# Performance work log

Measured on AMD Instinct MI355X. Metric: run time of the kernel, lower is better.

## Reference

```python
import jax, jax.numpy as jnp
import numpy as np

NUM_HEADS = 16

def setup_inputs() -> dict:
    key = jax.random.key(0)
    ks = jax.random.split(key, 6)
    b, t, d = 2, 2048, 1024
    s = 0.02
    return {
        "x": jax.random.normal(ks[0], (b, t, d), jnp.float32),
        "Wq": jax.random.normal(ks[1], (d, d), jnp.float32) * s,
        "Wk": jax.random.normal(ks[2], (d, d), jnp.float32) * s,
        "Wv": jax.random.normal(ks[3], (d, d), jnp.float32) * s,
        "Wo": jax.random.normal(ks[4], (d, d), jnp.float32) * s,
        "bo": jnp.zeros((d,), jnp.float32),
    }

def reference(x, Wq, Wk, Wv, Wo, bo):
    b, t, d = x.shape
    h = NUM_HEADS
    hd = d // h  # head_dim = d_out / num_heads
    # torch nn.Linear: y = x @ W.T (qkv_bias=False)
    def split_heads(y):
        return y.reshape(b, t, h, hd).transpose(0, 2, 1, 3)  # [b,h,t,hd]
    q = split_heads(x @ Wq.T)
    k = split_heads(x @ Wk.T)
    v = split_heads(x @ Wv.T)
    scale = 1.0 / jnp.sqrt(jnp.asarray(hd, x.dtype))
    # NOTE: original forward computes but never applies the causal mask or dropout
    scores = jnp.einsum('bhqd,bhkd->bhqk', q, k) * scale
    attn = jax.nn.softmax(scores, axis=-1)
    ctx = jnp.einsum('bhqk,bhkd->bhqd', attn, v)
    ctx = ctx.transpose(0, 2, 1, 3).reshape(b, t, d)
    return ctx @ Wo.T + bo
```

## Files before the change

### kernel.cpp

```cpp
#include <hip/hip_runtime.h>
#include <hip/hip_bf16.h>
#include <math.h>
#include <stdint.h>
#include <string.h>

#define TSEQ 2048
#define DMODEL 1024
#define NH 16
#define HD 64
#define BROWS 4096
#define BH 32

typedef __attribute__((ext_vector_type(8))) short short8;
typedef __attribute__((ext_vector_type(4))) float floatx4;

#define MFMA16 __builtin_amdgcn_mfma_f32_16x16x32_bf16
#define SWZ8(r, q) ((((q) ^ ((r) & 7)) * 8))

#define QSCALE 0.18033688011112042f

__device__ __forceinline__ unsigned short bf16_rne(float f) {
    uint32_t u = __float_as_uint(f);
    u += 0x7FFFu + ((u >> 16) & 1u);
    return (unsigned short)(u >> 16);
}

__device__ __forceinline__ uint32_t pack_bf16x2(float a, float b) {
    __hip_bfloat162 h = __float22bfloat162_rn(float2{a, b});
    uint32_t r;
    memcpy(&r, &h, 4);
    return r;
}

__device__ __forceinline__ void split_bf16(float f, short& hi, short& lo) {
    uint32_t u = __float_as_uint(f);
    hi = (short)(u >> 16);
    float hif = __uint_as_float(u & 0xFFFF0000u);
    lo = (short)bf16_rne(f - hif);
}

__device__ __forceinline__ void async16(const void* g, void* l) {
    __builtin_amdgcn_global_load_lds(
        (__attribute__((address_space(1))) const uint32_t*)g,
        (__attribute__((address_space(3))) uint32_t*)l, 16, 0, 0);
}

struct PackArgs {
    const float4* x;
    ushort4* xb;
    const float4* w[3];
    ushort4* wb[3];
    const float4* wo;
    ushort4* woh;
    ushort4* wol;
};
__global__ __launch_bounds__(256) void pack_all(PackArgs a) {
    const int y = blockIdx.y;
    const int base = blockIdx.x * 256 + threadIdx.x;
    if (y == 0) {
#pragma unroll
        for (int it = 0; it < 4; ++it) {
            int i = base + it * 262144;
            float4 f = a.x[i];
            a.xb[i] = make_ushort4(bf16_rne(f.x), bf16_rne(f.y),
                                   bf16_rne(f.z), bf16_rne(f.w));
        }
    } else if (y <= 3) {
        int w = y - 1;
        float4 f = a.w[w][base];
        a.wb[w][base] = make_ushort4(bf16_rne(f.x), bf16_rne(f.y),
                                     bf16_rne(f.z), bf16_rne(f.w));
    } else {
        float4 f = a.wo[base];
        short h0, l0, h1, l1, h2, l2, h3, l3;
        split_bf16(f.x, h0, l0); split_bf16(f.y, h1, l1);
        split_bf16(f.z, h2, l2); split_bf16(f.w, h3, l3);
        a.woh[base] = make_ushort4(h0, h1, h2, h3);
        a.wol[base] = make_ushort4(l0, l1, l2, l3);
    }
}

__global__ __launch_bounds__(256) void gemm_qkv(
    const short* __restrict__ Xb,
    const short* __restrict__ Bq, const short* __restrict__ Bk,
    const short* __restrict__ Bv,
    short* __restrict__ Qo, short* __restrict__ Ko, short* __restrict__ Vo) {
    __shared__ short sA[128 * 64];
    __shared__ short sB[128 * 64];
    const int K = DMODEL;

    const int tid = threadIdx.x;
    const int lane = tid & 63, wave = tid >> 6;
    const int quad = lane >> 4, col = lane & 15;
    const int m0 = blockIdx.y * 128, n0 = blockIdx.x * 128;
    const int which = n0 >> 10;
    const int nn0 = n0 & 1023;
    const int wm = wave >> 1, wn = wave & 1;

    const short* B = (which == 0) ? Bq : (which == 1) ? Bk : Bv;
    const short* Asrc = Xb + (size_t)m0 * K;
    const short* Bsrc = B + (size_t)nn0 * K;

    const int srow = lane >> 3;
    const int soff = (((lane & 7) ^ srow) * 8);

    floatx4 acc[4][4] = {};

    for (int k0 = 0; k0 < K; k0 += 64) {
        __syncthreads();
#pragma unroll
        for (int j = 0; j < 8; ++j) {
            int idx = wave * 8 + j;
            int sub = idx & 15;
            const short* s = (idx < 16) ? Asrc : Bsrc;
            short* d = (idx < 16) ? sA : sB;
            async16(s + (size_t)(sub * 8 + srow) * K + k0 + soff, d + sub * 512);
        }
        __syncthreads();

#pragma unroll
        for (int s2 = 0; s2 < 2; ++s2) {
            short8 a_b[4], b_b[4];
#pragma unroll
            for (int mi = 0; mi < 4; ++mi) {
                int r = wm * 64 + mi * 16 + col;
                a_b[mi] = *(const short8*)&sA[r * 64 + SWZ8(r, s2 * 4 + quad)];
            }
#pragma unroll
            for (int ni = 0; ni < 4; ++ni) {
                int r = wn * 64 + ni * 16 + col;
                b_b[ni] = *(const short8*)&sB[r * 64 + SWZ8(r, s2 * 4 + quad)];
            }
            if (which == 2) {
#pragma unroll
                for (int mi = 0; mi < 4; ++mi)
#pragma unroll
                    for (int ni = 0; ni < 4; ++ni)
                        acc[mi][ni] = MFMA16(a_b[mi], b_b[ni], acc[mi][ni], 0, 0, 0);
            } else {
#pragma unroll
                for (int mi = 0; mi < 4; ++mi)
#pragma unroll
                    for (int ni = 0; ni < 4; ++ni)
                        acc[mi][ni] = MFMA16(b_b[ni], a_b[mi], acc[mi][ni], 0, 0, 0);
            }
        }
    }

    const int mb = m0 + wm * 64;
    const int nlb = nn0 + wn * 64;
    if (which == 2) {
#pragma unroll
        for (int ni = 0; ni < 4; ++ni) {
            int n = nlb + ni * 16 + col;
            int h = n >> 6, hd = n & 63;
#pragma unroll
            for (int mi = 0; mi < 4; ++mi) {
                int m4 = mb + mi * 16 + quad * 4;
                int b = m4 >> 11, t0 = m4 & 2047;
                int sw = (t0 & 32) | ((t0 & 12) << 1) | ((t0 & 16) >> 2);
                int tsw = (t0 & ~63) | ((((sw >> 3) ^ (hd & 7)) << 3) | (sw & 7));
                size_t row = ((size_t)(b * NH + h) * HD + hd) * TSEQ;
                *(ushort4*)&Vo[row + tsw] =
                    make_ushort4(bf16_rne(acc[mi][ni][0]), bf16_rne(acc[mi][ni][1]),
                                 bf16_rne(acc[mi][ni][2]), bf16_rne(acc[mi][ni][3]));
            }
        }
    } else {
        short* O = (which == 0) ? Qo : Ko;
        const float sc = (which == 0) ? QSCALE : 1.0f;
#pragma unroll
        for (int mi = 0; mi < 4; ++mi) {
            int m = mb + mi * 16 + col;
            int b = m >> 11, t = m & 2047;
#pragma unroll
            for (int ni = 0; ni < 4; ++ni) {
                int n = nlb + ni * 16 + quad * 4;
                int h = n >> 6, hd = n & 63;
                int hds = (which == 1) ? ((((hd >> 3) ^ (t & 7)) << 3) | (hd & 7)) : hd;
                size_t idx = ((size_t)(b * NH + h) * TSEQ + t) * HD + hds;
                *(ushort4*)&O[idx] =
                    make_ushort4(bf16_rne(acc[mi][ni][0] * sc), bf16_rne(acc[mi][ni][1] * sc),
                                 bf16_rne(acc[mi][ni][2] * sc), bf16_rne(acc[mi][ni][3] * sc));
            }
        }
    }
}

#define ATTN_COMPUTE(DB)                                                        \
    {                                                                           \
        _Pragma("unroll")                                                       \
        for (int u = 0; u < 2; ++u) {                                           \
            floatx4 s[4] = {};                                                  \
            __builtin_amdgcn_s_setprio(1);                                      \
            _Pragma("unroll")                                                   \
            for (int k4 = 0; k4 < 4; ++k4) {                                    \
                short8 kf0 = *(const short8*)(kb0 + (DB) * 8192 + u * 4096 + k4 * 1024); \
                short8 kf1 = *(const short8*)(kb1 + (DB) * 8192 + u * 4096 + k4 * 1024); \
                s[k4] = MFMA16(kf0, qf[0], s[k4], 0, 0, 0);                     \
                s[k4] = MFMA16(kf1, qf[1], s[k4], 0, 0, 0);                     \
            }                                                                   \
            __builtin_amdgcn_s_setprio(0);                                      \
            float p[4][4];                                                      \
            _Pragma("unroll")                                                   \
            for (int k4 = 0; k4 < 4; ++k4)                                      \
                _Pragma("unroll")                                               \
                for (int r4 = 0; r4 < 4; ++r4)                                  \
                    p[k4][r4] = __builtin_amdgcn_exp2f(s[k4][r4]);              \
            _Pragma("unroll")                                                   \
            for (int c = 0; c < 2; ++c) {                                       \
                union { short8 v; uint32_t w[4]; } pf;                          \
                pf.w[0] = pack_bf16x2(p[2 * c][0], p[2 * c][1]);                \
                pf.w[1] = pack_bf16x2(p[2 * c][2], p[2 * c][3]);                \
                pf.w[2] = pack_bf16x2(p[2 * c + 1][0], p[2 * c + 1][1]);        \
                pf.w[3] = pack_bf16x2(p[2 * c + 1][2], p[2 * c + 1][3]);        \
                const short* vbc = c ? vb1 : vb0;                               \
                __builtin_amdgcn_s_setprio(1);                                  \
                lacc = MFMA16(ones.v, pf.v, lacc, 0, 0, 0);                     \
                _Pragma("unroll")                                               \
                for (int ni = 0; ni < 4; ++ni) {                                \
                    short8 vf = *(const short8*)(vbc + (DB) * 8192 + u * 4096 + ni * 1024); \
                    O[ni] = MFMA16(vf, pf.v, O[ni], 0, 0, 0);                   \
                }                                                               \
                __builtin_amdgcn_s_setprio(0);                                  \
            }                                                                   \
        }                                                                       \
    }

#define STAGE(LB)                                                               \
    {                                                                           \
        async16(g0, (LB) + 0 * 512);                                            \
        async16(g1, (LB) + 1 * 512);                                            \
        async16(g2, (LB) + 2 * 512);                                            \
        async16(g3, (LB) + 3 * 512);                                            \
        g0 += ktstep; g1 += ktstep; g2 += ktstep; g3 += ktstep;                 \
    }

__global__ __launch_bounds__(512, 4) void attn_bf16(
    const short* __restrict__ Qb, const short* __restrict__ Kb,
    const short* __restrict__ Vb, short* __restrict__ Cb) {
    __shared__ short sK[2][2][64 * 64];
    __shared__ short sV[2][2][64 * 64];

    const int tid = threadIdx.x;
    const int lane = tid & 63, wave = tid >> 6;
    const int quad = lane >> 4, col = lane & 15;
    const int qt = blockIdx.x, bh = blockIdx.y;
    const size_t bhoff = (size_t)bh * TSEQ * HD;

    const size_t qrow = (size_t)(qt * 128 + wave * 16 + col) * HD;
    short8 qf[2];
#pragma unroll
    for (int c = 0; c < 2; ++c)
        qf[c] = *(const short8*)&Qb[bhoff + qrow + c * 32 + quad * 8];

    const int srow = lane >> 3;
    const int schunk = (lane & 7) * 8;

    const int isV = wave >> 2;
    const int tl = (wave >> 1) & 1;
    const int sb = (wave & 1) * 4;

    const short *g0, *g1, *g2, *g3;
    size_t ktstep;
    if (!isV) {
        g0 = Kb + bhoff + (size_t)(tl * 64 + (sb + 0) * 8 + srow) * HD + schunk;
        g1 = Kb + bhoff + (size_t)(tl * 64 + (sb + 1) * 8 + srow) * HD + schunk;
        g2 = Kb + bhoff + (size_t)(tl * 64 + (sb + 2) * 8 + srow) * HD + schunk;
        g3 = Kb + bhoff + (size_t)(tl * 64 + (sb + 3) * 8 + srow) * HD + schunk;
        ktstep = (size_t)128 * HD;
    } else {
        g0 = Vb + bhoff + (size_t)((sb + 0) * 8 + srow) * TSEQ + tl * 64 + schunk;
        g1 = Vb + bhoff + (size_t)((sb + 1) * 8 + srow) * TSEQ + tl * 64 + schunk;
        g2 = Vb + bhoff + (size_t)((sb + 2) * 8 + srow) * TSEQ + tl * 64 + schunk;
        g3 = Vb + bhoff + (size_t)((sb + 3) * 8 + srow) * TSEQ + tl * 64 + schunk;
        ktstep = 128;
    }
    short* lb0_ = isV ? &sV[0][tl][sb * 512] : &sK[0][tl][sb * 512];
    short* lb1_ = isV ? &sV[1][tl][sb * 512] : &sK[1][tl][sb * 512];

    const int ch0 = ((quad ^ (col & 7)) << 3);
    const int ch1 = (((4 + quad) ^ (col & 7)) << 3);
    const short* kb0 = &sK[0][0][col * 64 + ch0];
    const short* kb1 = &sK[0][0][col * 64 + ch1];
    const short* vb0 = &sV[0][0][col * 64 + ch0];
    const short* vb1 = &sV[0][0][col * 64 + ch1];

    union { short8 v; short s[8]; } ones;
#pragma unroll
    for (int j = 0; j < 8; ++j) ones.s[j] = (short)0x3F80;

    floatx4 lacc = {};
    floatx4 O[4] = {};

    STAGE(lb0_);

    for (int kt2 = 0; kt2 < 8; ++kt2) {
        STAGE(lb1_);
        asm volatile("s_waitcnt vmcnt(4)" ::: "memory");
        __builtin_amdgcn_s_barrier();
        ATTN_COMPUTE(0);
        __builtin_amdgcn_s_barrier();

        if (kt2 < 7) {
            STAGE(lb0_);
            asm volatile("s_waitcnt vmcnt(4)" ::: "memory");
        } else {
            asm volatile("s_waitcnt vmcnt(0)" ::: "memory");
        }
        __builtin_amdgcn_s_barrier();
        ATTN_COMPUTE(1);
        __builtin_amdgcn_s_barrier();
    }

    const float inv = 1.0f / lacc[0];

    const int b = bh >> 4, h = bh & 15;
    const int trow = qt * 128 + wave * 16 + col;
    const size_t obase = (size_t)(b * TSEQ + trow) * DMODEL + h * 64;
#pragma unroll
    for (int ni = 0; ni < 4; ++ni) {
        uint2 pk;
        pk.x = pack_bf16x2(O[ni][0] * inv, O[ni][1] * inv);
        pk.y = pack_bf16x2(O[ni][2] * inv, O[ni][3] * inv);
        *(uint2*)&Cb[obase + ni * 16 + quad * 4] = pk;
    }
}

__global__ __launch_bounds__(256) void gemm_out(
    const short* __restrict__ Ab,
    const short* __restrict__ Bh, const short* __restrict__ Bl,
    const float* __restrict__ bias, float* __restrict__ Of) {
    __shared__ short sA[128 * 64];
    __shared__ short sBh[64 * 64];
    __shared__ short sBl[64 * 64];
    const int K = DMODEL, N = DMODEL;

    const int tid = threadIdx.x;
    const int lane = tid & 63, wave = tid >> 6;
    const int quad = lane >> 4, col = lane & 15;
    const int m0 = blockIdx.y * 128, n0 = blockIdx.x * 64;
    const int wm = wave >> 1, wn = wave & 1;

    const short* Asrc = Ab + (size_t)m0 * K;
    const short* Bhsrc = Bh + (size_t)n0 * K;
    const short* Blsrc = Bl + (size_t)n0 * K;
    const int srow = lane >> 3;
    const int soff = (((lane & 7) ^ srow) * 8);

    floatx4 acc[4][2] = {};

    for (int k0 = 0; k0 < K; k0 += 64) {
        __syncthreads();
#pragma unroll
        for (int j = 0; j < 8; ++j) {
            int idx = wave * 8 + j;
            int buf = (idx < 16) ? 0 : (idx < 24) ? 1 : 2;
            int sub = (buf == 0) ? idx : (buf == 1) ? idx - 16 : idx - 24;
            const short* s = (buf == 0) ? Asrc : (buf == 1) ? Bhsrc : Blsrc;
            short* d = (buf == 0) ? sA : (buf == 1) ? sBh : sBl;
            async16(s + (size_t)(sub * 8 + srow) * K + k0 + soff, d + sub * 512);
        }
        __syncthreads();

#pragma unroll
        for (int s2 = 0; s2 < 2; ++s2) {
            short8 a_b[4], b_h[2], b_l[2];
#pragma unroll
            for (int mi = 0; mi < 4; ++mi) {
                int r = wm * 64 + mi * 16 + col;
                a_b[mi] = *(const short8*)&sA[r * 64 + SWZ8(r, s2 * 4 + quad)];
            }
#pragma unroll
            for (int ni = 0; ni < 2; ++ni) {
                int r = wn * 32 + ni * 16 + col;
                b_h[ni] = *(const short8*)&sBh[r * 64 + SWZ8(r, s2 * 4 + quad)];
                b_l[ni] = *(const short8*)&sBl[r * 64 + SWZ8(r, s2 * 4 + quad)];
            }
#pragma unroll
            for (int mi = 0; mi < 4; ++mi)
#pragma unroll
                for (int ni = 0; ni < 2; ++ni) {
                    acc[mi][ni] = MFMA16(b_h[ni], a_b[mi], acc[mi][ni], 0, 0, 0);
                    acc[mi][ni] = MFMA16(b_l[ni], a_b[mi], acc[mi][ni], 0, 0, 0);
                }
        }
    }

    const int mb = m0 + wm * 64, nb = n0 + wn * 32;
#pragma unroll
    for (int mi = 0; mi < 4; ++mi) {
        int m = mb + mi * 16 + col;
#pragma unroll
        for (int ni = 0; ni < 2; ++ni) {
            int n = nb + ni * 16 + quad * 4;
            float4 bv = *(const float4*)&bias[n];
            float4 o = make_float4(acc[mi][ni][0] + bv.x, acc[mi][ni][1] + bv.y,
                                   acc[mi][ni][2] + bv.z, acc[mi][ni][3] + bv.w);
            *(float4*)&Of[(size_t)m * N + n] = o;
        }
    }
}

extern "C" void kernel_launch(void* const* d_in, const int* in_sizes, int n_in,
                              void* d_out, int out_size, void* d_ws, size_t ws_size,
                              hipStream_t stream) {
    const float* x  = (const float*)d_in[0];
    const float* Wq = (const float*)d_in[1];
    const float* Wk = (const float*)d_in[2];
    const float* Wv = (const float*)d_in[3];
    const float* Wo = (const float*)d_in[4];
    const float* bo = (const float*)d_in[5];
    float* out = (float*)d_out;

    const size_t NX = (size_t)BROWS * DMODEL;
    const size_t NW = (size_t)DMODEL * DMODEL;
    short* p = (short*)d_ws;
    short *xb = p;
    short *wqb = xb + NX;
    short *wkb = wqb + NW;
    short *wvb = wkb + NW;
    short *woh = wvb + NW; short *wol = woh + NW;
    short *qb = wol + NW;
    short *kb = qb + NX;
    short *vb = kb + NX;
    short *cb = vb + NX;

    PackArgs pa;
    pa.x = (const float4*)x; pa.xb = (ushort4*)xb;
    pa.w[0] = (const float4*)Wq; pa.wb[0] = (ushort4*)wqb;
    pa.w[1] = (const float4*)Wk; pa.wb[1] = (ushort4*)wkb;
    pa.w[2] = (const float4*)Wv; pa.wb[2] = (ushort4*)wvb;
    pa.wo = (const float4*)Wo; pa.woh = (ushort4*)woh; pa.wol = (ushort4*)wol;
    pack_all<<<dim3(1024, 5), dim3(256), 0, stream>>>(pa);

    gemm_qkv<<<dim3(3 * DMODEL / 128, BROWS / 128), dim3(256), 0, stream>>>(
        xb, wqb, wkb, wvb, qb, kb, vb);

    attn_bf16<<<dim3(TSEQ / 128, BH), dim3(512), 0, stream>>>(qb, kb, vb, cb);

    gemm_out<<<dim3(DMODEL / 64, BROWS / 128), dim3(256), 0, stream>>>(cb, woh, wol, bo, out);
}
```

Before: 196.4 us.

## Switch attention kernel to 32x32x16 MFMA tiles with 4 waves per block

Rewrites the attention inner loop to use 32x32x16 bf16 MFMA instead of 16x16x32. Each wave now owns 32 query rows, and the block drops from 8 waves to 4. The softmax row sum is now accumulated in VALU and finished with a cross-lane shuffle, replacing the ones-vector MFMA. The V layout swizzle written by the QKV GEMM and the K/V staging loop are changed to match the new fragment layout. Larger MFMA tiles should raise LDS operand reuse and cut instruction count, at the cost of more registers per wave and fewer waves to hide latency.

```diff
diff --git a/kernel.cpp b/kernel.cpp
--- a/kernel.cpp
+++ b/kernel.cpp
@@ -13,8 +13,10 @@
 
 typedef __attribute__((ext_vector_type(8))) short short8;
 typedef __attribute__((ext_vector_type(4))) float floatx4;
+typedef __attribute__((ext_vector_type(16))) float floatx16;
 
 #define MFMA16 __builtin_amdgcn_mfma_f32_16x16x32_bf16
+#define MFMA32 __builtin_amdgcn_mfma_f32_32x32x16_bf16
 #define SWZ8(r, q) ((((q) ^ ((r) & 7)) * 8))
 
 #define QSCALE 0.18033688011112042f
@@ -158,7 +160,7 @@
             for (int mi = 0; mi < 4; ++mi) {
                 int m4 = mb + mi * 16 + quad * 4;
                 int b = m4 >> 11, t0 = m4 & 2047;
-                int sw = (t0 & 32) | ((t0 & 12) << 1) | ((t0 & 16) >> 2);
+                int sw = (t0 & 0x33) | ((t0 & 4) << 1) | ((t0 & 8) >> 1);
                 int tsw = (t0 & ~63) | ((((sw >> 3) ^ (hd & 7)) << 3) | (sw & 7));
                 size_t row = ((size_t)(b * NH + h) * HD + hd) * TSEQ;
                 *(ushort4*)&Vo[row + tsw] =
@@ -189,38 +191,39 @@
 
 #define ATTN_COMPUTE(DB)                                                        \
     {                                                                           \
+        floatx16 s[4] = {};                                                     \
+        __builtin_amdgcn_s_setprio(1);                                          \
         _Pragma("unroll")                                                       \
-        for (int u = 0; u < 2; ++u) {                                           \
-            floatx4 s[4] = {};                                                  \
-            __builtin_amdgcn_s_setprio(1);                                      \
+        for (int u = 0; u < 2; ++u)                                             \
             _Pragma("unroll")                                                   \
-            for (int k4 = 0; k4 < 4; ++k4) {                                    \
-                short8 kf0 = *(const short8*)(kb0 + (DB) * 8192 + u * 4096 + k4 * 1024); \
-                short8 kf1 = *(const short8*)(kb1 + (DB) * 8192 + u * 4096 + k4 * 1024); \
-                s[k4] = MFMA16(kf0, qf[0], s[k4], 0, 0, 0);                     \
-                s[k4] = MFMA16(kf1, qf[1], s[k4], 0, 0, 0);                     \
+            for (int mm = 0; mm < 2; ++mm)                                      \
+                _Pragma("unroll")                                               \
+                for (int ks = 0; ks < 4; ++ks) {                                \
+                    short8 kf = *(const short8*)(kB[ks] + (DB) * 8192 + u * 4096 + mm * 2048); \
+                    s[u * 2 + mm] = MFMA32(kf, qf[ks], s[u * 2 + mm], 0, 0, 0); \
+                }                                                               \
+        __builtin_amdgcn_s_setprio(0);                                          \
+        _Pragma("unroll")                                                       \
+        for (int m = 0; m < 4; ++m) {                                           \
+            float p[16];                                                        \
+            _Pragma("unroll")                                                   \
+            for (int r = 0; r < 16; ++r) {                                      \
+                p[r] = __builtin_amdgcn_exp2f(s[m][r]);                         \
+                lv[r & 3] += p[r];                                              \
             }                                                                   \
-            __builtin_amdgcn_s_setprio(0);                                      \
-            float p[4][4];                                                      \
-            _Pragma("unroll")                                                   \
-            for (int k4 = 0; k4 < 4; ++k4)                                      \
-                _Pragma("unroll")                                               \
-                for (int r4 = 0; r4 < 4; ++r4)                                  \
-                    p[k4][r4] = __builtin_amdgcn_exp2f(s[k4][r4]);              \
             _Pragma("unroll")                                                   \
             for (int c = 0; c < 2; ++c) {                                       \
                 union { short8 v; uint32_t w[4]; } pf;                          \
-                pf.w[0] = pack_bf16x2(p[2 * c][0], p[2 * c][1]);                \
-                pf.w[1] = pack_bf16x2(p[2 * c][2], p[2 * c][3]);                \
-                pf.w[2] = pack_bf16x2(p[2 * c + 1][0], p[2 * c + 1][1]);        \
-                pf.w[3] = pack_bf16x2(p[2 * c + 1][2], p[2 * c + 1][3]);        \
-                const short* vbc = c ? vb1 : vb0;                               \
+                pf.w[0] = pack_bf16x2(p[8 * c + 0], p[8 * c + 1]);              \
+                pf.w[1] = pack_bf16x2(p[8 * c + 2], p[8 * c + 3]);              \
+                pf.w[2] = pack_bf16x2(p[8 * c + 4], p[8 * c + 5]);              \
+                pf.w[3] = pack_bf16x2(p[8 * c + 6], p[8 * c + 7]);              \
+                const int t = m * 2 + c, uu = t >> 2, tt = t & 3;               \
                 __builtin_amdgcn_s_setprio(1);                                  \
-                lacc = MFMA16(ones.v, pf.v, lacc, 0, 0, 0);                     \
                 _Pragma("unroll")                                               \
-                for (int ni = 0; ni < 4; ++ni) {                                \
-                    short8 vf = *(const short8*)(vbc + (DB) * 8192 + u * 4096 + ni * 1024); \
-                    O[ni] = MFMA16(vf, pf.v, O[ni], 0, 0, 0);                   \
+                for (int mi = 0; mi < 2; ++mi) {                                \
+                    short8 vf = *(const short8*)(vB[tt] + (DB) * 8192 + uu * 4096 + mi * 2048); \
+                    O2[mi] = MFMA32(vf, pf.v, O2[mi], 0, 0, 0);                 \
                 }                                                               \
                 __builtin_amdgcn_s_setprio(0);                                  \
             }                                                                   \
@@ -229,14 +232,13 @@
 
 #define STAGE(LB)                                                               \
     {                                                                           \
-        async16(g0, (LB) + 0 * 512);                                            \
-        async16(g1, (LB) + 1 * 512);                                            \
-        async16(g2, (LB) + 2 * 512);                                            \
-        async16(g3, (LB) + 3 * 512);                                            \
-        g0 += ktstep; g1 += ktstep; g2 += ktstep; g3 += ktstep;                 \
-    }
-
-__global__ __launch_bounds__(512, 4) void attn_bf16(
+        _Pragma("unroll")                                                       \
+        for (int j = 0; j < 8; ++j)                                             \
+            async16(gb + (size_t)j * gstride, (LB) + j * 512);                  \
+        gb += ktstep;                                                           \
+    }
+
+__global__ __launch_bounds__(256, 2) void attn_bf16(
     const short* __restrict__ Qb, const short* __restrict__ Kb,
     const short* __restrict__ Vb, short* __restrict__ Cb) {
     __shared__ short sK[2][2][64 * 64];
@@ -244,67 +246,55 @@
 
     const int tid = threadIdx.x;
     const int lane = tid & 63, wave = tid >> 6;
-    const int quad = lane >> 4, col = lane & 15;
+    const int q5 = lane & 31, hh = lane >> 5, l7 = lane & 7;
     const int qt = blockIdx.x, bh = blockIdx.y;
     const size_t bhoff = (size_t)bh * TSEQ * HD;
 
-    const size_t qrow = (size_t)(qt * 128 + wave * 16 + col) * HD;
-    short8 qf[2];
-#pragma unroll
-    for (int c = 0; c < 2; ++c)
-        qf[c] = *(const short8*)&Qb[bhoff + qrow + c * 32 + quad * 8];
-
-    const int srow = lane >> 3;
-    const int schunk = (lane & 7) * 8;
-
-    const int isV = wave >> 2;
-    const int tl = (wave >> 1) & 1;
-    const int sb = (wave & 1) * 4;
-
-    const short *g0, *g1, *g2, *g3;
-    size_t ktstep;
+    const size_t qrow = (size_t)(qt * 128 + wave * 32 + q5) * HD;
+    short8 qf[4];
+#pragma unroll
+    for (int ks = 0; ks < 4; ++ks)
+        qf[ks] = *(const short8*)&Qb[bhoff + qrow + ks * 16 + hh * 8];
+
+    const int srow = lane >> 3, schunk = (lane & 7) * 8;
+    const int isV = wave >> 1, tl = wave & 1;
+    const short* gb;
+    size_t gstride, ktstep;
     if (!isV) {
-        g0 = Kb + bhoff + (size_t)(tl * 64 + (sb + 0) * 8 + srow) * HD + schunk;
-        g1 = Kb + bhoff + (size_t)(tl * 64 + (sb + 1) * 8 + srow) * HD + schunk;
-        g2 = Kb + bhoff + (size_t)(tl * 64 + (sb + 2) * 8 + srow) * HD + schunk;
-        g3 = Kb + bhoff + (size_t)(tl * 64 + (sb + 3) * 8 + srow) * HD + schunk;
+        gb = Kb + bhoff + (size_t)(tl * 64 + srow) * HD + schunk;
+        gstride = (size_t)8 * HD;
         ktstep = (size_t)128 * HD;
     } else {
-        g0 = Vb + bhoff + (size_t)((sb + 0) * 8 + srow) * TSEQ + tl * 64 + schunk;
-        g1 = Vb + bhoff + (size_t)((sb + 1) * 8 + srow) * TSEQ + tl * 64 + schunk;
-        g2 = Vb + bhoff + (size_t)((sb + 2) * 8 + srow) * TSEQ + tl * 64 + schunk;
-        g3 = Vb + bhoff + (size_t)((sb + 3) * 8 + srow) * TSEQ + tl * 64 + schunk;
+        gb = Vb + bhoff + (size_t)srow * TSEQ + tl * 64 + schunk;
+        gstride = (size_t)8 * TSEQ;
         ktstep = 128;
     }
-    short* lb0_ = isV ? &sV[0][tl][sb * 512] : &sK[0][tl][sb * 512];
-    short* lb1_ = isV ? &sV[1][tl][sb * 512] : &sK[1][tl][sb * 512];
-
-    const int ch0 = ((quad ^ (col & 7)) << 3);
-    const int ch1 = (((4 + quad) ^ (col & 7)) << 3);
-    const short* kb0 = &sK[0][0][col * 64 + ch0];
-    const short* kb1 = &sK[0][0][col * 64 + ch1];
-    const short* vb0 = &sV[0][0][col * 64 + ch0];
-    const short* vb1 = &sV[0][0][col * 64 + ch1];
-
-    union { short8 v; short s[8]; } ones;
-#pragma unroll
-    for (int j = 0; j < 8; ++j) ones.s[j] = (short)0x3F80;
-
-    floatx4 lacc = {};
-    floatx4 O[4] = {};
-
-    STAGE(lb0_);
+    short* lb0 = isV ? sV[0][tl] : sK[0][tl];
+    short* lb1 = isV ? sV[1][tl] : sK[1][tl];
+
+    const short* kB[4];
+    const short* vB[4];
+#pragma unroll
+    for (int w = 0; w < 4; ++w) {
+        kB[w] = &sK[0][0][q5 * 64 + (((2 * w + hh) ^ l7) * 8)];
+        vB[w] = &sV[0][0][q5 * 64 + (((2 * w + hh) ^ l7) * 8)];
+    }
+
+    floatx4 lv = {};
+    floatx16 O2[2] = {};
+
+    STAGE(lb0);
 
     for (int kt2 = 0; kt2 < 8; ++kt2) {
-        STAGE(lb1_);
-        asm volatile("s_waitcnt vmcnt(4)" ::: "memory");
+        STAGE(lb1);
+        asm volatile("s_waitcnt vmcnt(8)" ::: "memory");
         __builtin_amdgcn_s_barrier();
         ATTN_COMPUTE(0);
         __builtin_amdgcn_s_barrier();
 
         if (kt2 < 7) {
-            STAGE(lb0_);
-            asm volatile("s_waitcnt vmcnt(4)" ::: "memory");
+            STAGE(lb0);
+            asm volatile("s_waitcnt vmcnt(8)" ::: "memory");
         } else {
             asm volatile("s_waitcnt vmcnt(0)" ::: "memory");
         }
@@ -313,18 +303,22 @@
         __builtin_amdgcn_s_barrier();
     }
 
-    const float inv = 1.0f / lacc[0];
+    float l_r = (lv[0] + lv[1]) + (lv[2] + lv[3]);
+    l_r += __shfl_xor(l_r, 32);
+    const float inv = 1.0f / l_r;
 
     const int b = bh >> 4, h = bh & 15;
-    const int trow = qt * 128 + wave * 16 + col;
+    const int trow = qt * 128 + wave * 32 + q5;
     const size_t obase = (size_t)(b * TSEQ + trow) * DMODEL + h * 64;
 #pragma unroll
-    for (int ni = 0; ni < 4; ++ni) {
-        uint2 pk;
-        pk.x = pack_bf16x2(O[ni][0] * inv, O[ni][1] * inv);
-        pk.y = pack_bf16x2(O[ni][2] * inv, O[ni][3] * inv);
-        *(uint2*)&Cb[obase + ni * 16 + quad * 4] = pk;
-    }
+    for (int mi = 0; mi < 2; ++mi)
+#pragma unroll
+        for (int g = 0; g < 4; ++g) {
+            uint2 pk;
+            pk.x = pack_bf16x2(O2[mi][4 * g + 0] * inv, O2[mi][4 * g + 1] * inv);
+            pk.y = pack_bf16x2(O2[mi][4 * g + 2] * inv, O2[mi][4 * g + 3] * inv);
+            *(uint2*)&Cb[obase + mi * 32 + g * 8 + hh * 4] = pk;
+        }
 }
 
 __global__ __launch_bounds__(256) void gemm_out(
@@ -437,7 +431,7 @@
     gemm_qkv<<<dim3(3 * DMODEL / 128, BROWS / 128), dim3(256), 0, stream>>>(
         xb, wqb, wkb, wvb, qb, kb, vb);
 
-    attn_bf16<<<dim3(TSEQ / 128, BH), dim3(512), 0, stream>>>(qb, kb, vb, cb);
+    attn_bf16<<<dim3(TSEQ / 128, BH), dim3(256), 0, stream>>>(qb, kb, vb, cb);
 
     gemm_out<<<dim3(DMODEL / 64, BROWS / 128), dim3(256), 0, stream>>>(cb, woh, wol, bo, out);
 }
```

Measured after the change: 192.8 us. Within noise of the previous version (-1.8%).

## Triple-buffer QKV GEMM with async prefetch and 256x128 tiles

Applied to the files above, without the earlier changes.

Rewrites the QKV projection GEMM to use a three-stage shared-memory ring: global-to-LDS async loads for the tile two steps ahead are issued while the MFMAs for the current tile run. Blocks now cover 256 rows with 512 threads (8 waves), which halves the grid and reuses each B tile across more rows. Fragments are loaded into registers before the loads for the next stage are issued, and MFMAs run at raised priority. The cost is more LDS per block (about 144 KB) and fewer resident blocks, plus a fully unrolled main loop that relies on K being fixed at 1024.

```diff
diff --git a/kernel.cpp b/kernel.cpp
--- a/kernel.cpp
+++ b/kernel.cpp
@@ -80,19 +80,74 @@
     }
 }
 
-__global__ __launch_bounds__(256) void gemm_qkv(
+#define QSTG(SB)                                                                \
+    {                                                                           \
+        async16(ga0, &sA[SB][(subA + 0) * 512]); ga0 += 64;                     \
+        async16(ga1, &sA[SB][(subA + 1) * 512]); ga1 += 64;                     \
+        async16(ga2, &sA[SB][(subA + 2) * 512]); ga2 += 64;                     \
+        async16(ga3, &sA[SB][(subA + 3) * 512]); ga3 += 64;                     \
+        async16(gb0, &sB[SB][(subB + 0) * 512]); gb0 += 64;                     \
+        async16(gb1, &sB[SB][(subB + 1) * 512]); gb1 += 64;                     \
+    }
+
+#define QSTEP(C, SB, STG, VM)                                                   \
+    {                                                                           \
+        asm volatile("s_waitcnt vmcnt(" #VM ")" ::: "memory");                  \
+        __builtin_amdgcn_s_barrier();                                           \
+        __builtin_amdgcn_sched_barrier(0);                                      \
+        short8 a_b[2][4], b_b[2][4];                                            \
+        _Pragma("unroll")                                                       \
+        for (int s2 = 0; s2 < 2; ++s2) {                                        \
+            _Pragma("unroll")                                                   \
+            for (int mi = 0; mi < 4; ++mi) {                                    \
+                int r = wm * 64 + mi * 16 + col;                                \
+                a_b[s2][mi] = *(const short8*)&sA[C][r * 64 + SWZ8(r, s2 * 4 + quad)]; \
+            }                                                                   \
+            _Pragma("unroll")                                                   \
+            for (int ni = 0; ni < 4; ++ni) {                                    \
+                int r = wn * 64 + ni * 16 + col;                                \
+                b_b[s2][ni] = *(const short8*)&sB[C][r * 64 + SWZ8(r, s2 * 4 + quad)]; \
+            }                                                                   \
+        }                                                                       \
+        asm volatile("s_waitcnt lgkmcnt(0)" ::: "memory");                      \
+        __builtin_amdgcn_sched_barrier(0);                                      \
+        __builtin_amdgcn_s_barrier();                                           \
+        __builtin_amdgcn_sched_barrier(0);                                      \
+        if (STG) QSTG(SB);                                                      \
+        __builtin_amdgcn_s_setprio(1);                                          \
+        if (which == 2) {                                                       \
+            _Pragma("unroll")                                                   \
+            for (int s2 = 0; s2 < 2; ++s2)                                      \
+                _Pragma("unroll")                                               \
+                for (int mi = 0; mi < 4; ++mi)                                  \
+                    _Pragma("unroll")                                           \
+                    for (int ni = 0; ni < 4; ++ni)                              \
+                        acc[mi][ni] = MFMA16(a_b[s2][mi], b_b[s2][ni], acc[mi][ni], 0, 0, 0); \
+        } else {                                                                \
+            _Pragma("unroll")                                                   \
+            for (int s2 = 0; s2 < 2; ++s2)                                      \
+                _Pragma("unroll")                                               \
+                for (int mi = 0; mi < 4; ++mi)                                  \
+                    _Pragma("unroll")                                           \
+                    for (int ni = 0; ni < 4; ++ni)                              \
+                        acc[mi][ni] = MFMA16(b_b[s2][ni], a_b[s2][mi], acc[mi][ni], 0, 0, 0); \
+        }                                                                       \
+        __builtin_amdgcn_s_setprio(0);                                          \
+    }
+
+__global__ __launch_bounds__(512, 2) void gemm_qkv(
     const short* __restrict__ Xb,
     const short* __restrict__ Bq, const short* __restrict__ Bk,
     const short* __restrict__ Bv,
     short* __restrict__ Qo, short* __restrict__ Ko, short* __restrict__ Vo) {
-    __shared__ short sA[128 * 64];
-    __shared__ short sB[128 * 64];
+    __shared__ short sA[3][256 * 64];
+    __shared__ short sB[3][128 * 64];
     const int K = DMODEL;
 
     const int tid = threadIdx.x;
     const int lane = tid & 63, wave = tid >> 6;
     const int quad = lane >> 4, col = lane & 15;
-    const int m0 = blockIdx.y * 128, n0 = blockIdx.x * 128;
+    const int m0 = blockIdx.y * 256, n0 = blockIdx.x * 128;
     const int which = n0 >> 10;
     const int nn0 = n0 & 1023;
     const int wm = wave >> 1, wn = wave & 1;
@@ -104,48 +159,35 @@
     const int srow = lane >> 3;
     const int soff = (((lane & 7) ^ srow) * 8);
 
+    const int subA = wave * 4, subB = wave * 2;
+    const short* ga0 = Asrc + (size_t)((subA + 0) * 8 + srow) * K + soff;
+    const short* ga1 = Asrc + (size_t)((subA + 1) * 8 + srow) * K + soff;
+    const short* ga2 = Asrc + (size_t)((subA + 2) * 8 + srow) * K + soff;
+    const short* ga3 = Asrc + (size_t)((subA + 3) * 8 + srow) * K + soff;
+    const short* gb0 = Bsrc + (size_t)((subB + 0) * 8 + srow) * K + soff;
+    const short* gb1 = Bsrc + (size_t)((subB + 1) * 8 + srow) * K + soff;
+
     floatx4 acc[4][4] = {};
 
-    for (int k0 = 0; k0 < K; k0 += 64) {
-        __syncthreads();
-#pragma unroll
-        for (int j = 0; j < 8; ++j) {
-            int idx = wave * 8 + j;
-            int sub = idx & 15;
-            const short* s = (idx < 16) ? Asrc : Bsrc;
-            short* d = (idx < 16) ? sA : sB;
-            async16(s + (size_t)(sub * 8 + srow) * K + k0 + soff, d + sub * 512);
-        }
-        __syncthreads();
-
-#pragma unroll
-        for (int s2 = 0; s2 < 2; ++s2) {
-            short8 a_b[4], b_b[4];
-#pragma unroll
-            for (int mi = 0; mi < 4; ++mi) {
-                int r = wm * 64 + mi * 16 + col;
-                a_b[mi] = *(const short8*)&sA[r * 64 + SWZ8(r, s2 * 4 + quad)];
-            }
-#pragma unroll
-            for (int ni = 0; ni < 4; ++ni) {
-                int r = wn * 64 + ni * 16 + col;
-                b_b[ni] = *(const short8*)&sB[r * 64 + SWZ8(r, s2 * 4 + quad)];
-            }
-            if (which == 2) {
-#pragma unroll
-                for (int mi = 0; mi < 4; ++mi)
-#pragma unroll
-                    for (int ni = 0; ni < 4; ++ni)
-                        acc[mi][ni] = MFMA16(a_b[mi], b_b[ni], acc[mi][ni], 0, 0, 0);
-            } else {
-#pragma unroll
-                for (int mi = 0; mi < 4; ++mi)
-#pragma unroll
-                    for (int ni = 0; ni < 4; ++ni)
-                        acc[mi][ni] = MFMA16(b_b[ni], a_b[mi], acc[mi][ni], 0, 0, 0);
-            }
-        }
-    }
+    QSTG(0);
+    QSTG(1);
+
+    QSTEP(0, 2, 1, 6);
+    QSTEP(1, 0, 1, 6);
+    QSTEP(2, 1, 1, 6);
+    QSTEP(0, 2, 1, 6);
+    QSTEP(1, 0, 1, 6);
+    QSTEP(2, 1, 1, 6);
+    QSTEP(0, 2, 1, 6);
+    QSTEP(1, 0, 1, 6);
+    QSTEP(2, 1, 1, 6);
+    QSTEP(0, 2, 1, 6);
+    QSTEP(1, 0, 1, 6);
+    QSTEP(2, 1, 1, 6);
+    QSTEP(0, 2, 1, 6);
+    QSTEP(1, 0, 1, 6);
+    QSTEP(2, 1, 0, 6);
+    QSTEP(0, 2, 0, 0);
 
     const int mb = m0 + wm * 64;
     const int nlb = nn0 + wn * 64;
@@ -227,7 +269,7 @@
         }                                                                       \
     }
 
-#define STAGE(LB)                                                               \
+#define ASTAGE(LB)                                                              \
     {                                                                           \
         async16(g0, (LB) + 0 * 512);                                            \
         async16(g1, (LB) + 1 * 512);                                            \
@@ -293,17 +335,17 @@
     floatx4 lacc = {};
     floatx4 O[4] = {};
 
-    STAGE(lb0_);
+    ASTAGE(lb0_);
 
     for (int kt2 = 0; kt2 < 8; ++kt2) {
-        STAGE(lb1_);
+        ASTAGE(lb1_);
         asm volatile("s_waitcnt vmcnt(4)" ::: "memory");
         __builtin_amdgcn_s_barrier();
         ATTN_COMPUTE(0);
         __builtin_amdgcn_s_barrier();
 
         if (kt2 < 7) {
-            STAGE(lb0_);
+            ASTAGE(lb0_);
             asm volatile("s_waitcnt vmcnt(4)" ::: "memory");
         } else {
             asm volatile("s_waitcnt vmcnt(0)" ::: "memory");
@@ -434,7 +476,7 @@
     pa.wo = (const float4*)Wo; pa.woh = (ushort4*)woh; pa.wol = (ushort4*)wol;
     pack_all<<<dim3(1024, 5), dim3(256), 0, stream>>>(pa);
 
-    gemm_qkv<<<dim3(3 * DMODEL / 128, BROWS / 128), dim3(256), 0, stream>>>(
+    gemm_qkv<<<dim3(3 * DMODEL / 128, BROWS / 256), dim3(512), 0, stream>>>(
         xb, wqb, wkb, wvb, qb, kb, vb);
 
     attn_bf16<<<dim3(TSEQ / 128, BH), dim3(512), 0, stream>>>(qb, kb, vb, cb);
```

New measurement: 190.8 us. -2.8%, faster.

## Double-buffer GEMM tiles and remap blocks for XCD-aware L2 locality

Applied to the files above, without the earlier changes.

The QKV and output-projection GEMMs now double-buffer their LDS tiles. The next K-slice is prefetched asynchronously while MFMAs run on the current one, and wave priority is raised around the MFMA block. All three kernels remap the linear block index so that blocks landing on the same XCD share the same rows or heads, which is meant to improve L2 reuse. The double buffering doubles LDS use per block and could lower occupancy.

```diff
diff --git a/kernel.cpp b/kernel.cpp
--- a/kernel.cpp
+++ b/kernel.cpp
@@ -80,19 +80,36 @@
     }
 }
 
+#define QSTAGE(DB, K0)                                                          \
+    {                                                                           \
+        _Pragma("unroll")                                                       \
+        for (int j = 0; j < 8; ++j) {                                           \
+            int idx = wave * 8 + j;                                             \
+            int sub = idx & 15;                                                 \
+            const short* s = (idx < 16) ? Asrc : Bsrc;                          \
+            short* d = (idx < 16) ? sA[DB] : sB[DB];                            \
+            async16(s + (size_t)(sub * 8 + srow) * K + (K0) + soff, d + sub * 512); \
+        }                                                                       \
+    }
+
 __global__ __launch_bounds__(256) void gemm_qkv(
     const short* __restrict__ Xb,
     const short* __restrict__ Bq, const short* __restrict__ Bk,
     const short* __restrict__ Bv,
     short* __restrict__ Qo, short* __restrict__ Ko, short* __restrict__ Vo) {
-    __shared__ short sA[128 * 64];
-    __shared__ short sB[128 * 64];
+    __shared__ short sA[2][128 * 64];
+    __shared__ short sB[2][128 * 64];
     const int K = DMODEL;
 
     const int tid = threadIdx.x;
     const int lane = tid & 63, wave = tid >> 6;
     const int quad = lane >> 4, col = lane & 15;
-    const int m0 = blockIdx.y * 128, n0 = blockIdx.x * 128;
+
+    const int lin = blockIdx.y * 24 + blockIdx.x;
+    const int xcd = lin & 7, j8 = lin >> 3;
+    const int bxp = 3 * xcd + (j8 % 3);
+    const int byp = j8 / 3;
+    const int m0 = byp * 128, n0 = bxp * 128;
     const int which = n0 >> 10;
     const int nn0 = n0 & 1023;
     const int wm = wave >> 1, wn = wave & 1;
@@ -106,17 +123,16 @@
 
     floatx4 acc[4][4] = {};
 
-    for (int k0 = 0; k0 < K; k0 += 64) {
-        __syncthreads();
-#pragma unroll
-        for (int j = 0; j < 8; ++j) {
-            int idx = wave * 8 + j;
-            int sub = idx & 15;
-            const short* s = (idx < 16) ? Asrc : Bsrc;
-            short* d = (idx < 16) ? sA : sB;
-            async16(s + (size_t)(sub * 8 + srow) * K + k0 + soff, d + sub * 512);
-        }
-        __syncthreads();
+    QSTAGE(0, 0);
+    for (int t = 0; t < 16; ++t) {
+        const int db = t & 1;
+        if (t < 15) {
+            QSTAGE(db ^ 1, (t + 1) * 64);
+            asm volatile("s_waitcnt vmcnt(8)" ::: "memory");
+        } else {
+            asm volatile("s_waitcnt vmcnt(0)" ::: "memory");
+        }
+        __builtin_amdgcn_s_barrier();
 
 #pragma unroll
         for (int s2 = 0; s2 < 2; ++s2) {
@@ -124,13 +140,14 @@
 #pragma unroll
             for (int mi = 0; mi < 4; ++mi) {
                 int r = wm * 64 + mi * 16 + col;
-                a_b[mi] = *(const short8*)&sA[r * 64 + SWZ8(r, s2 * 4 + quad)];
+                a_b[mi] = *(const short8*)&sA[db][r * 64 + SWZ8(r, s2 * 4 + quad)];
             }
 #pragma unroll
             for (int ni = 0; ni < 4; ++ni) {
                 int r = wn * 64 + ni * 16 + col;
-                b_b[ni] = *(const short8*)&sB[r * 64 + SWZ8(r, s2 * 4 + quad)];
-            }
+                b_b[ni] = *(const short8*)&sB[db][r * 64 + SWZ8(r, s2 * 4 + quad)];
+            }
+            __builtin_amdgcn_s_setprio(1);
             if (which == 2) {
 #pragma unroll
                 for (int mi = 0; mi < 4; ++mi)
@@ -144,7 +161,9 @@
                     for (int ni = 0; ni < 4; ++ni)
                         acc[mi][ni] = MFMA16(b_b[ni], a_b[mi], acc[mi][ni], 0, 0, 0);
             }
-        }
+            __builtin_amdgcn_s_setprio(0);
+        }
+        __builtin_amdgcn_s_barrier();
     }
 
     const int mb = m0 + wm * 64;
@@ -227,7 +246,7 @@
         }                                                                       \
     }
 
-#define STAGE(LB)                                                               \
+#define ASTAGE(LB)                                                              \
     {                                                                           \
         async16(g0, (LB) + 0 * 512);                                            \
         async16(g1, (LB) + 1 * 512);                                            \
@@ -245,7 +264,11 @@
     const int tid = threadIdx.x;
     const int lane = tid & 63, wave = tid >> 6;
     const int quad = lane >> 4, col = lane & 15;
-    const int qt = blockIdx.x, bh = blockIdx.y;
+
+    const int lin = blockIdx.y * 16 + blockIdx.x;
+    const int xcd = lin & 7, j8 = lin >> 3;
+    const int qt = j8 & 15;
+    const int bh = 4 * xcd + (j8 >> 4);
     const size_t bhoff = (size_t)bh * TSEQ * HD;
 
     const size_t qrow = (size_t)(qt * 128 + wave * 16 + col) * HD;
@@ -293,17 +316,17 @@
     floatx4 lacc = {};
     floatx4 O[4] = {};
 
-    STAGE(lb0_);
+    ASTAGE(lb0_);
 
     for (int kt2 = 0; kt2 < 8; ++kt2) {
-        STAGE(lb1_);
+        ASTAGE(lb1_);
         asm volatile("s_waitcnt vmcnt(4)" ::: "memory");
         __builtin_amdgcn_s_barrier();
         ATTN_COMPUTE(0);
         __builtin_amdgcn_s_barrier();
 
         if (kt2 < 7) {
-            STAGE(lb0_);
+            ASTAGE(lb0_);
             asm volatile("s_waitcnt vmcnt(4)" ::: "memory");
         } else {
             asm volatile("s_waitcnt vmcnt(0)" ::: "memory");
@@ -327,19 +350,37 @@
     }
 }
 
+#define OSTAGE(DB, K0)                                                          \
+    {                                                                           \
+        _Pragma("unroll")                                                       \
+        for (int j = 0; j < 8; ++j) {                                           \
+            int idx = wave * 8 + j;                                             \
+            int buf = (idx < 16) ? 0 : (idx < 24) ? 1 : 2;                      \
+            int sub = (buf == 0) ? idx : (buf == 1) ? idx - 16 : idx - 24;      \
+            const short* s = (buf == 0) ? Asrc : (buf == 1) ? Bhsrc : Blsrc;    \
+            short* d = (buf == 0) ? sA[DB] : (buf == 1) ? sBh[DB] : sBl[DB];    \
+            async16(s + (size_t)(sub * 8 + srow) * K + (K0) + soff, d + sub * 512); \
+        }                                                                       \
+    }
+
 __global__ __launch_bounds__(256) void gemm_out(
     const short* __restrict__ Ab,
     const short* __restrict__ Bh, const short* __restrict__ Bl,
     const float* __restrict__ bias, float* __restrict__ Of) {
-    __shared__ short sA[128 * 64];
-    __shared__ short sBh[64 * 64];
-    __shared__ short sBl[64 * 64];
+    __shared__ short sA[2][128 * 64];
+    __shared__ short sBh[2][64 * 64];
+    __shared__ short sBl[2][64 * 64];
     const int K = DMODEL, N = DMODEL;
 
     const int tid = threadIdx.x;
     const int lane = tid & 63, wave = tid >> 6;
     const int quad = lane >> 4, col = lane & 15;
-    const int m0 = blockIdx.y * 128, n0 = blockIdx.x * 64;
+
+    const int lin = blockIdx.y * 16 + blockIdx.x;
+    const int xcd = lin & 7, j8 = lin >> 3;
+    const int bxp = 2 * xcd + (j8 & 1);
+    const int byp = j8 >> 1;
+    const int m0 = byp * 128, n0 = bxp * 64;
     const int wm = wave >> 1, wn = wave & 1;
 
     const short* Asrc = Ab + (size_t)m0 * K;
@@ -350,18 +391,16 @@
 
     floatx4 acc[4][2] = {};
 
-    for (int k0 = 0; k0 < K; k0 += 64) {
-        __syncthreads();
-#pragma unroll
-        for (int j = 0; j < 8; ++j) {
-            int idx = wave * 8 + j;
-            int buf = (idx < 16) ? 0 : (idx < 24) ? 1 : 2;
-            int sub = (buf == 0) ? idx : (buf == 1) ? idx - 16 : idx - 24;
-            const short* s = (buf == 0) ? Asrc : (buf == 1) ? Bhsrc : Blsrc;
-            short* d = (buf == 0) ? sA : (buf == 1) ? sBh : sBl;
-            async16(s + (size_t)(sub * 8 + srow) * K + k0 + soff, d + sub * 512);
-        }
-        __syncthreads();
+    OSTAGE(0, 0);
+    for (int t = 0; t < 16; ++t) {
+        const int db = t & 1;
+        if (t < 15) {
+            OSTAGE(db ^ 1, (t + 1) * 64);
+            asm volatile("s_waitcnt vmcnt(8)" ::: "memory");
+        } else {
+            asm volatile("s_waitcnt vmcnt(0)" ::: "memory");
+        }
+        __builtin_amdgcn_s_barrier();
 
 #pragma unroll
         for (int s2 = 0; s2 < 2; ++s2) {
@@ -369,14 +408,15 @@
 #pragma unroll
             for (int mi = 0; mi < 4; ++mi) {
                 int r = wm * 64 + mi * 16 + col;
-                a_b[mi] = *(const short8*)&sA[r * 64 + SWZ8(r, s2 * 4 + quad)];
+                a_b[mi] = *(const short8*)&sA[db][r * 64 + SWZ8(r, s2 * 4 + quad)];
             }
 #pragma unroll
             for (int ni = 0; ni < 2; ++ni) {
                 int r = wn * 32 + ni * 16 + col;
-                b_h[ni] = *(const short8*)&sBh[r * 64 + SWZ8(r, s2 * 4 + quad)];
-                b_l[ni] = *(const short8*)&sBl[r * 64 + SWZ8(r, s2 * 4 + quad)];
-            }
+                b_h[ni] = *(const short8*)&sBh[db][r * 64 + SWZ8(r, s2 * 4 + quad)];
+                b_l[ni] = *(const short8*)&sBl[db][r * 64 + SWZ8(r, s2 * 4 + quad)];
+            }
+            __builtin_amdgcn_s_setprio(1);
 #pragma unroll
             for (int mi = 0; mi < 4; ++mi)
 #pragma unroll
@@ -384,7 +424,9 @@
                     acc[mi][ni] = MFMA16(b_h[ni], a_b[mi], acc[mi][ni], 0, 0, 0);
                     acc[mi][ni] = MFMA16(b_l[ni], a_b[mi], acc[mi][ni], 0, 0, 0);
                 }
-        }
+            __builtin_amdgcn_s_setprio(0);
+        }
+        __builtin_amdgcn_s_barrier();
     }
 
     const int mb = m0 + wm * 64, nb = n0 + wn * 32;
```

Result: faster. 183.0 us (-6.8%).
